# Performance work log

Measured on AMD Instinct MI355X. Metric: run time of the kernel, lower is better.

## Reference

```python
import jax, jax.numpy as jnp
import numpy as np

B, K, T = 64, 256, 64      # batch, num_tokens (feature dim of e / Dense units), word tokens
DF, N = 768, 1024          # image feature channels, spatial regions


def setup_inputs() -> dict:
    key = jax.random.key(0)
    k1, k2, k3 = jax.random.split(key, 3)
    e = jax.random.normal(k1, (B, K, T), dtype=jnp.float32)
    f = jax.random.normal(k2, (B, DF, N), dtype=jnp.float32)
    # Dense(units=K) kernel/bias (Glorot-ish scale)
    W = jax.random.normal(k3, (DF, K), dtype=jnp.float32) / np.sqrt(DF)
    b = jnp.zeros((K,), dtype=jnp.float32)
    gamma = jnp.float32(5.0)  # DAMSM smoothing factor gamma1
    return {"e": e, "f": f, "gamma": gamma, "W": W, "b": b}


def reference(e, f, gamma, W, b):
    # v = transpose(Dense(transpose(f))): project image features Df -> K. [B,K,N]
    v = jnp.einsum('bdn,dk->bkn', f, W) + b[None, :, None]
    # attention scores between word tokens and regions: [B,T,N]
    s = jnp.einsum('bkt,bkn->btn', e, v)
    # gamma-scaled softmax over regions (axis=2)
    alpha = jax.nn.softmax(gamma * s, axis=2)
    # region-context vectors per token: [B,K,T]
    c = jnp.einsum('bkn,btn->bkt', v, alpha)
    # per-token feature norms (reduce over feature axis 1): [B,T]
    lc = jnp.sqrt(jnp.sum(c * c, axis=1))
    le = jnp.sqrt(jnp.sum(e * e, axis=1))
    # token-token cosine similarity: contract feature axis, normalize by outer(lc, le)
    cos = jnp.einsum('bki,bkj->bij', c, e) / (lc[:, :, None] * le[:, None, :])
    return cos
```

## Files before the change

kernel.cpp:

```cpp
#include <hip/hip_runtime.h>

#define B_  64
#define K_  256
#define T_  64
#define DF_ 768
#define N_  1024

typedef __attribute__((ext_vector_type(8))) short bf16x8;
typedef __attribute__((ext_vector_type(4))) float f32x4;

__device__ __forceinline__ unsigned short bf_rne(float x) {
    unsigned u = __float_as_uint(x);
    unsigned r = u + 0x7fffu + ((u >> 16) & 1u);
    return (unsigned short)(r >> 16);
}

__global__ __launch_bounds__(256) void prep_we(const float* __restrict__ W,
                                               const float* __restrict__ e,
                                               unsigned short* __restrict__ W_hi,
                                               unsigned short* __restrict__ W_lo,
                                               unsigned short* __restrict__ WT_hi,
                                               unsigned short* __restrict__ eT_hi,
                                               unsigned short* __restrict__ eT_lo) {
    int blk = blockIdx.x;
    if (blk < DF_) {
        int d = blk, k = threadIdx.x;
        float w = W[d * K_ + k];
        unsigned u = __float_as_uint(w);
        unsigned short hs = (unsigned short)(u >> 16);
        float hi = __uint_as_float(u & 0xffff0000u);
        W_hi[d * K_ + k]   = hs;
        W_lo[d * K_ + k]   = bf_rne(w - hi);
        WT_hi[k * DF_ + d] = hs;
    } else {
        int q = blk - DF_;
        int b = q >> 2, kq = q & 3;
        int t = threadIdx.x & 63, ko = threadIdx.x >> 6;
        const float* eb = e + (size_t)b * K_ * T_;
        unsigned short* eh = eT_hi + (size_t)b * T_ * K_;
        unsigned short* el = eT_lo + (size_t)b * T_ * K_;
#pragma unroll
        for (int i = 0; i < 16; i++) {
            int k = kq * 64 + ko * 16 + i;
            float x = eb[k * T_ + t];
            unsigned u = __float_as_uint(x);
            unsigned short hs = (unsigned short)(u >> 16);
            float hi = __uint_as_float(u & 0xffff0000u);
            eh[t * K_ + k] = hs;
            el[t * K_ + k] = bf_rne(x - hi);
        }
    }
}

__global__ __launch_bounds__(256, 2) void gemm_g(const unsigned short* __restrict__ eT_hi,
                                                 const unsigned short* __restrict__ eT_lo,
                                                 const unsigned short* __restrict__ W_hi,
                                                 const unsigned short* __restrict__ W_lo,
                                                 unsigned short* __restrict__ gT_hi,
                                                 unsigned short* __restrict__ gT_lo) {
    __shared__ unsigned short LeH[64 * 40], LeL[64 * 40];
    __shared__ unsigned short LwH[64 * 40], LwL[64 * 40];
    const int dblk = blockIdx.x * 64;
    const int b = blockIdx.y;
    const int tid = threadIdx.x;
    const int lane = tid & 63, w = tid >> 6, q = lane >> 4, l16 = lane & 15;

    const unsigned short* eh = eT_hi + (size_t)b * T_ * K_;
    const unsigned short* el = eT_lo + (size_t)b * T_ * K_;

    f32x4 acc[4];
#pragma unroll
    for (int i = 0; i < 4; i++) acc[i] = (f32x4)(0.f);

    const int tr = tid >> 2, c8 = (tid & 3) * 8;
    for (int k0 = 0; k0 < K_; k0 += 32) {
        *(uint4*)&LeH[tr * 40 + c8] = *(const uint4*)&eh[tr * K_ + k0 + c8];
        *(uint4*)&LeL[tr * 40 + c8] = *(const uint4*)&el[tr * K_ + k0 + c8];
        *(uint4*)&LwH[tr * 40 + c8] = *(const uint4*)&W_hi[(size_t)(dblk + tr) * K_ + k0 + c8];
        *(uint4*)&LwL[tr * 40 + c8] = *(const uint4*)&W_lo[(size_t)(dblk + tr) * K_ + k0 + c8];
        __syncthreads();
        bf16x8 aH[4], aL[4], bH, bL;
#pragma unroll
        for (int mt = 0; mt < 4; mt++) {
            aH[mt] = *(const bf16x8*)&LeH[(mt * 16 + l16) * 40 + q * 8];
            aL[mt] = *(const bf16x8*)&LeL[(mt * 16 + l16) * 40 + q * 8];
        }
        int dl = w * 16 + l16;
        bH = *(const bf16x8*)&LwH[dl * 40 + q * 8];
        bL = *(const bf16x8*)&LwL[dl * 40 + q * 8];
#pragma unroll
        for (int mt = 0; mt < 4; mt++) {
            acc[mt] = __builtin_amdgcn_mfma_f32_16x16x32_bf16(aH[mt], bH, acc[mt], 0, 0, 0);
            acc[mt] = __builtin_amdgcn_mfma_f32_16x16x32_bf16(aH[mt], bL, acc[mt], 0, 0, 0);
            acc[mt] = __builtin_amdgcn_mfma_f32_16x16x32_bf16(aL[mt], bH, acc[mt], 0, 0, 0);
        }
        __syncthreads();
    }

    unsigned short* gh = gT_hi + (size_t)b * T_ * DF_;
    unsigned short* gl = gT_lo + (size_t)b * T_ * DF_;
#pragma unroll
    for (int mt = 0; mt < 4; mt++)
#pragma unroll
        for (int r = 0; r < 4; r++) {
            float x = acc[mt][r];
            int t = mt * 16 + q * 4 + r;
            int d = dblk + w * 16 + l16;
            unsigned u = __float_as_uint(x);
            unsigned short hs = (unsigned short)(u >> 16);
            float hi = __uint_as_float(u & 0xffff0000u);
            gh[t * DF_ + d] = hs;
            gl[t * DF_ + d] = bf_rne(x - hi);
        }
}

__global__ __launch_bounds__(256, 2) void gemm_s(const unsigned short* __restrict__ gT_hi,
                                                 const unsigned short* __restrict__ gT_lo,
                                                 const float* __restrict__ f,
                                                 float* __restrict__ s) {
    __shared__ unsigned short LgH[64 * 40], LgL[64 * 40];
    __shared__ unsigned LfH[128 * 20], LfL[128 * 20];

    const int flat = blockIdx.x;
    const int b    = (flat & 7) * 8 + ((flat >> 3) & 7);
    const int nblk = (flat >> 6) * 128;
    const int tid = threadIdx.x;
    const int lane = tid & 63, w = tid >> 6, q = lane >> 4, l16 = lane & 15;

    const unsigned short* gh = gT_hi + (size_t)b * T_ * DF_;
    const unsigned short* gl = gT_lo + (size_t)b * T_ * DF_;

    f32x4 acc[4][2];
#pragma unroll
    for (int i = 0; i < 4; i++)
#pragma unroll
        for (int j = 0; j < 2; j++) acc[i][j] = (f32x4)(0.f);

    const int dp  = tid >> 4;
    const int nb  = (tid & 15) * 8;
    const int rot = tid & 7;
    const int tr = tid >> 2, c8 = (tid & 3) * 8;

    for (int d0 = 0; d0 < DF_; d0 += 32) {
        *(uint4*)&LgH[tr * 40 + c8] = *(const uint4*)&gh[tr * DF_ + d0 + c8];
        *(uint4*)&LgL[tr * 40 + c8] = *(const uint4*)&gl[tr * DF_ + d0 + c8];
        {
            const float* fp = f + ((size_t)b * DF_ + d0 + dp * 2) * N_ + nblk + nb;
            float4 x0 = *(const float4*)&fp[0];
            float4 x1 = *(const float4*)&fp[4];
            float4 y0 = *(const float4*)&fp[N_ + 0];
            float4 y1 = *(const float4*)&fp[N_ + 4];
            const float xs[8] = {x0.x, x0.y, x0.z, x0.w, x1.x, x1.y, x1.z, x1.w};
            const float ys[8] = {y0.x, y0.y, y0.z, y0.w, y1.x, y1.y, y1.z, y1.w};
#pragma unroll
            for (int jj = 0; jj < 8; jj++) {
                int j = (jj + rot) & 7;
                unsigned bx = __float_as_uint(xs[j]);
                unsigned by = __float_as_uint(ys[j]);
                unsigned hp = (bx >> 16) | (by & 0xffff0000u);
                float lx = xs[j] - __uint_as_float(bx & 0xffff0000u);
                float ly = ys[j] - __uint_as_float(by & 0xffff0000u);
                unsigned lp = (__float_as_uint(lx) >> 16) | (__float_as_uint(ly) & 0xffff0000u);
                LfH[(nb + j) * 20 + dp] = hp;
                LfL[(nb + j) * 20 + dp] = lp;
            }
        }
        __syncthreads();
        bf16x8 aH[4], aL[4], bH[2], bL[2];
#pragma unroll
        for (int mt = 0; mt < 4; mt++) {
            aH[mt] = *(const bf16x8*)&LgH[(mt * 16 + l16) * 40 + q * 8];
            aL[mt] = *(const bf16x8*)&LgL[(mt * 16 + l16) * 40 + q * 8];
        }
#pragma unroll
        for (int nt = 0; nt < 2; nt++) {
            int nl = w * 32 + nt * 16 + l16;
            bH[nt] = *(const bf16x8*)&((const unsigned short*)LfH)[nl * 40 + q * 8];
            bL[nt] = *(const bf16x8*)&((const unsigned short*)LfL)[nl * 40 + q * 8];
        }
#pragma unroll
        for (int mt = 0; mt < 4; mt++)
#pragma unroll
            for (int nt = 0; nt < 2; nt++) {
                acc[mt][nt] = __builtin_amdgcn_mfma_f32_16x16x32_bf16(aH[mt], bH[nt], acc[mt][nt], 0, 0, 0);
                acc[mt][nt] = __builtin_amdgcn_mfma_f32_16x16x32_bf16(aH[mt], bL[nt], acc[mt][nt], 0, 0, 0);
                acc[mt][nt] = __builtin_amdgcn_mfma_f32_16x16x32_bf16(aL[mt], bH[nt], acc[mt][nt], 0, 0, 0);
            }
        __syncthreads();
    }

    float* sb = s + (size_t)b * T_ * N_;
#pragma unroll
    for (int mt = 0; mt < 4; mt++)
#pragma unroll
        for (int nt = 0; nt < 2; nt++)
#pragma unroll
            for (int r = 0; r < 4; r++) {
                int t = mt * 16 + q * 4 + r;
                int n = nblk + w * 32 + nt * 16 + l16;
                sb[(size_t)t * N_ + n] = acc[mt][nt][r];
            }
}

__global__ __launch_bounds__(256) void softmax_k(const float* __restrict__ s,
                                                 unsigned short* __restrict__ alpha,
                                                 const float* __restrict__ gptr) {
    const float g = gptr[0];
    const float* row = s + (size_t)blockIdx.x * N_;
    unsigned short* arow = alpha + (size_t)blockIdx.x * N_;
    const int t = threadIdx.x;

    float4 x = *(const float4*)(row + t * 4);
    x.x *= g; x.y *= g; x.z *= g; x.w *= g;

    float m = fmaxf(fmaxf(x.x, x.y), fmaxf(x.z, x.w));
#pragma unroll
    for (int off = 32; off > 0; off >>= 1) m = fmaxf(m, __shfl_xor(m, off, 64));
    __shared__ float sm[4], ss[4];
    int wave = t >> 6;
    if ((t & 63) == 0) sm[wave] = m;
    __syncthreads();
    m = fmaxf(fmaxf(sm[0], sm[1]), fmaxf(sm[2], sm[3]));

    float e0 = __expf(x.x - m), e1 = __expf(x.y - m);
    float e2 = __expf(x.z - m), e3 = __expf(x.w - m);
    float sum = e0 + e1 + e2 + e3;
#pragma unroll
    for (int off = 32; off > 0; off >>= 1) sum += __shfl_xor(sum, off, 64);
    if ((t & 63) == 0) ss[wave] = sum;
    __syncthreads();
    sum = ss[0] + ss[1] + ss[2] + ss[3];
    float inv = 1.f / sum;
    unsigned p0 = (unsigned)bf_rne(e0 * inv) | ((unsigned)bf_rne(e1 * inv) << 16);
    unsigned p1 = (unsigned)bf_rne(e2 * inv) | ((unsigned)bf_rne(e3 * inv) << 16);
    uint2 o; o.x = p0; o.y = p1;
    *(uint2*)&arow[t * 4] = o;
}

__global__ __launch_bounds__(256, 2) void gemm_h(const float* __restrict__ f,
                                                 const unsigned short* __restrict__ alpha,
                                                 unsigned short* __restrict__ hT) {
    __shared__ unsigned short Lf[64 * 72];
    __shared__ unsigned short La[64 * 72];
    const int dblk = blockIdx.x * 64;
    const int b = blockIdx.y;
    const int tid = threadIdx.x;
    const int lane = tid & 63, w = tid >> 6, q = lane >> 4, l16 = lane & 15;

    const float* fb = f + (size_t)b * DF_ * N_;
    const unsigned short* ab = alpha + (size_t)b * T_ * N_;

    f32x4 acc[4];
#pragma unroll
    for (int i = 0; i < 4; i++) acc[i] = (f32x4)(0.f);

    const int fr_ = tid >> 2, fc = tid & 3;
    for (int n0 = 0; n0 < N_; n0 += 64) {
        const float* frp = fb + (size_t)(dblk + fr_) * N_ + n0 + fc * 16;
#pragma unroll
        for (int i = 0; i < 4; i++) {
            float4 x = *(const float4*)&frp[i * 4];
            unsigned p0 = (unsigned)bf_rne(x.x) | ((unsigned)bf_rne(x.y) << 16);
            unsigned p1 = (unsigned)bf_rne(x.z) | ((unsigned)bf_rne(x.w) << 16);
            uint2 o; o.x = p0; o.y = p1;
            *(uint2*)&Lf[fr_ * 72 + fc * 16 + i * 4] = o;
        }
#pragma unroll
        for (int l = 0; l < 2; l++) {
            int idx = tid * 2 + l;
            int r = idx >> 3, c8 = (idx & 7) * 8;
            *(uint4*)&La[r * 72 + c8] = *(const uint4*)&ab[(size_t)r * N_ + n0 + c8];
        }
        __syncthreads();
        bf16x8 af[2], bb[4][2];
#pragma unroll
        for (int kk = 0; kk < 2; kk++)
            af[kk] = *(const bf16x8*)&Lf[(w * 16 + l16) * 72 + kk * 32 + q * 8];
#pragma unroll
        for (int nt = 0; nt < 4; nt++)
#pragma unroll
            for (int kk = 0; kk < 2; kk++)
                bb[nt][kk] = *(const bf16x8*)&La[(nt * 16 + l16) * 72 + kk * 32 + q * 8];
#pragma unroll
        for (int nt = 0; nt < 4; nt++)
#pragma unroll
            for (int kk = 0; kk < 2; kk++)
                acc[nt] = __builtin_amdgcn_mfma_f32_16x16x32_bf16(af[kk], bb[nt][kk], acc[nt], 0, 0, 0);
        __syncthreads();
    }

    unsigned short* hb = hT + (size_t)b * T_ * DF_;
#pragma unroll
    for (int nt = 0; nt < 4; nt++)
#pragma unroll
        for (int r = 0; r < 4; r++) {
            int d = dblk + w * 16 + q * 4 + r;
            int t = nt * 16 + l16;
            hb[(size_t)t * DF_ + d] = bf_rne(acc[nt][r]);
        }
}

__global__ __launch_bounds__(256, 2) void gemm_c(const unsigned short* __restrict__ WT_hi,
                                                 const unsigned short* __restrict__ hT,
                                                 const float* __restrict__ bias,
                                                 float* __restrict__ c) {
    __shared__ unsigned short LW[64 * 72];
    __shared__ unsigned short Lh[64 * 72];
    const int kblk = blockIdx.x * 64;
    const int b = blockIdx.y;
    const int tid = threadIdx.x;
    const int lane = tid & 63, w = tid >> 6, q = lane >> 4, l16 = lane & 15;

    const unsigned short* hb = hT + (size_t)b * T_ * DF_;

    f32x4 acc[4];
#pragma unroll
    for (int i = 0; i < 4; i++) acc[i] = (f32x4)(0.f);

    for (int d0 = 0; d0 < DF_; d0 += 64) {
#pragma unroll
        for (int l = 0; l < 2; l++) {
            int idx = tid * 2 + l;
            int r = idx >> 3, c8 = (idx & 7) * 8;
            *(uint4*)&LW[r * 72 + c8] = *(const uint4*)&WT_hi[(size_t)(kblk + r) * DF_ + d0 + c8];
            *(uint4*)&Lh[r * 72 + c8] = *(const uint4*)&hb[(size_t)r * DF_ + d0 + c8];
        }
        __syncthreads();
        bf16x8 aw[2], bh[4][2];
#pragma unroll
        for (int kk = 0; kk < 2; kk++)
            aw[kk] = *(const bf16x8*)&LW[(w * 16 + l16) * 72 + kk * 32 + q * 8];
#pragma unroll
        for (int nt = 0; nt < 4; nt++)
#pragma unroll
            for (int kk = 0; kk < 2; kk++)
                bh[nt][kk] = *(const bf16x8*)&Lh[(nt * 16 + l16) * 72 + kk * 32 + q * 8];
#pragma unroll
        for (int nt = 0; nt < 4; nt++)
#pragma unroll
            for (int kk = 0; kk < 2; kk++)
                acc[nt] = __builtin_amdgcn_mfma_f32_16x16x32_bf16(aw[kk], bh[nt][kk], acc[nt], 0, 0, 0);
        __syncthreads();
    }

    float* cb = c + (size_t)b * K_ * T_;
#pragma unroll
    for (int nt = 0; nt < 4; nt++)
#pragma unroll
        for (int r = 0; r < 4; r++) {
            int k = kblk + w * 16 + q * 4 + r;
            int t = nt * 16 + l16;
            cb[(size_t)k * T_ + t] = acc[nt][r] + bias[k];
        }
}

__global__ __launch_bounds__(256) void cos_k(const float* __restrict__ c,
                                             const float* __restrict__ e,
                                             float* __restrict__ out) {
    const int iq = threadIdx.x >> 6;
    const int i = blockIdx.x * 4 + iq;
    const int b = blockIdx.y;
    const int j = threadIdx.x & 63;
    const float* cb = c + (size_t)b * K_ * T_;
    const float* eb = e + (size_t)b * K_ * T_;

    float dot = 0.f, se = 0.f, sc = 0.f;
#pragma unroll 8
    for (int k = 0; k < K_; k++) {
        float cv = cb[(size_t)k * T_ + i];
        float ev = eb[(size_t)k * T_ + j];
        dot += cv * ev;
        se  += ev * ev;
        sc  += cv * cv;
    }
    out[((size_t)b * T_ + i) * T_ + j] = dot * rsqrtf(sc * se);
}

extern "C" void kernel_launch(void* const* d_in, const int* in_sizes, int n_in,
                              void* d_out, int out_size, void* d_ws, size_t ws_size,
                              hipStream_t stream) {
    const float* e     = (const float*)d_in[0];
    const float* f     = (const float*)d_in[1];
    const float* gamma = (const float*)d_in[2];
    const float* W     = (const float*)d_in[3];
    const float* bias  = (const float*)d_in[4];
    float* out = (float*)d_out;

    char* p = (char*)d_ws;
    unsigned short* W_hi  = (unsigned short*)p; p += (size_t)DF_ * K_ * 2;
    unsigned short* W_lo  = (unsigned short*)p; p += (size_t)DF_ * K_ * 2;
    unsigned short* WT_hi = (unsigned short*)p; p += (size_t)DF_ * K_ * 2;
    unsigned short* eT_hi = (unsigned short*)p; p += (size_t)B_ * T_ * K_ * 2;
    unsigned short* eT_lo = (unsigned short*)p; p += (size_t)B_ * T_ * K_ * 2;
    unsigned short* gT_hi = (unsigned short*)p; p += (size_t)B_ * T_ * DF_ * 2;
    unsigned short* gT_lo = (unsigned short*)p; p += (size_t)B_ * T_ * DF_ * 2;
    float*          s     = (float*)p;          p += (size_t)B_ * T_ * N_ * 4;
    unsigned short* alpha = (unsigned short*)p; p += (size_t)B_ * T_ * N_ * 2;
    unsigned short* hT    = (unsigned short*)p; p += (size_t)B_ * T_ * DF_ * 2;
    float*          c     = (float*)p;          p += (size_t)B_ * K_ * T_ * 4;

    prep_we <<<dim3(DF_ + 256),     256, 0, stream>>>(W, e, W_hi, W_lo, WT_hi, eT_hi, eT_lo);
    gemm_g  <<<dim3(DF_ / 64, B_),  256, 0, stream>>>(eT_hi, eT_lo, W_hi, W_lo, gT_hi, gT_lo);
    gemm_s  <<<dim3(512),           256, 0, stream>>>(gT_hi, gT_lo, f, s);
    softmax_k<<<dim3(B_ * T_),      256, 0, stream>>>(s, alpha, gamma);
    gemm_h  <<<dim3(DF_ / 64, B_),  256, 0, stream>>>(f, alpha, hT);
    gemm_c  <<<dim3(K_ / 64, B_),   256, 0, stream>>>(WT_hi, hT, bias, c);
    cos_k   <<<dim3(T_ / 4, B_),    256, 0, stream>>>(c, e, out);
}
```

Baseline: 383.5 us.

## Register-prefetch global loads in GEMM kernels and use one wave per softmax row

Adds register double-buffering to the gemm_g, gemm_s, gemm_h and gemm_c main loops. Each loop loads the next tile's global data into registers while the current tile is computed from LDS, so global memory latency is overlapped with MFMA work. The softmax kernel now assigns one wavefront per row, four rows per block, which removes the LDS cross-wave reductions and block barriers. Launch bounds for gemm_g and gemm_h are raised to 3 blocks per CU. The extra live prefetch registers may force spills or lower occupancy under that tighter register budget.

```diff
diff --git a/kernel.cpp b/kernel.cpp
--- a/kernel.cpp
+++ b/kernel.cpp
@@ -52,7 +52,7 @@
     }
 }
 
-__global__ __launch_bounds__(256, 2) void gemm_g(const unsigned short* __restrict__ eT_hi,
+__global__ __launch_bounds__(256, 3) void gemm_g(const unsigned short* __restrict__ eT_hi,
                                                  const unsigned short* __restrict__ eT_lo,
                                                  const unsigned short* __restrict__ W_hi,
                                                  const unsigned short* __restrict__ W_lo,
@@ -73,12 +73,27 @@
     for (int i = 0; i < 4; i++) acc[i] = (f32x4)(0.f);
 
     const int tr = tid >> 2, c8 = (tid & 3) * 8;
-    for (int k0 = 0; k0 < K_; k0 += 32) {
-        *(uint4*)&LeH[tr * 40 + c8] = *(const uint4*)&eh[tr * K_ + k0 + c8];
-        *(uint4*)&LeL[tr * 40 + c8] = *(const uint4*)&el[tr * K_ + k0 + c8];
-        *(uint4*)&LwH[tr * 40 + c8] = *(const uint4*)&W_hi[(size_t)(dblk + tr) * K_ + k0 + c8];
-        *(uint4*)&LwL[tr * 40 + c8] = *(const uint4*)&W_lo[(size_t)(dblk + tr) * K_ + k0 + c8];
-        __syncthreads();
+    const unsigned short* ehp = eh + (size_t)tr * K_ + c8;
+    const unsigned short* elp = el + (size_t)tr * K_ + c8;
+    const unsigned short* whp = W_hi + (size_t)(dblk + tr) * K_ + c8;
+    const unsigned short* wlp = W_lo + (size_t)(dblk + tr) * K_ + c8;
+
+    struct GSet { uint4 eH, eL, wH, wL; };
+    GSet A, Bv;
+
+    auto gload = [&](GSet& S, int k0) {
+        S.eH = *(const uint4*)&ehp[k0];
+        S.eL = *(const uint4*)&elp[k0];
+        S.wH = *(const uint4*)&whp[k0];
+        S.wL = *(const uint4*)&wlp[k0];
+    };
+    auto gstore = [&](const GSet& S) {
+        *(uint4*)&LeH[tr * 40 + c8] = S.eH;
+        *(uint4*)&LeL[tr * 40 + c8] = S.eL;
+        *(uint4*)&LwH[tr * 40 + c8] = S.wH;
+        *(uint4*)&LwL[tr * 40 + c8] = S.wL;
+    };
+    auto gcomp = [&]() {
         bf16x8 aH[4], aL[4], bH, bL;
 #pragma unroll
         for (int mt = 0; mt < 4; mt++) {
@@ -94,6 +109,19 @@
             acc[mt] = __builtin_amdgcn_mfma_f32_16x16x32_bf16(aH[mt], bL, acc[mt], 0, 0, 0);
             acc[mt] = __builtin_amdgcn_mfma_f32_16x16x32_bf16(aL[mt], bH, acc[mt], 0, 0, 0);
         }
+    };
+
+    gload(A, 0);
+    for (int k0 = 0; k0 < K_; k0 += 64) {
+        gload(Bv, k0 + 32);
+        gstore(A);
+        __syncthreads();
+        gcomp();
+        __syncthreads();
+        if (k0 + 64 < K_) gload(A, k0 + 64);
+        gstore(Bv);
+        __syncthreads();
+        gcomp();
         __syncthreads();
     }
 
@@ -141,31 +169,41 @@
     const int rot = tid & 7;
     const int tr = tid >> 2, c8 = (tid & 3) * 8;
 
-    for (int d0 = 0; d0 < DF_; d0 += 32) {
-        *(uint4*)&LgH[tr * 40 + c8] = *(const uint4*)&gh[tr * DF_ + d0 + c8];
-        *(uint4*)&LgL[tr * 40 + c8] = *(const uint4*)&gl[tr * DF_ + d0 + c8];
-        {
-            const float* fp = f + ((size_t)b * DF_ + d0 + dp * 2) * N_ + nblk + nb;
-            float4 x0 = *(const float4*)&fp[0];
-            float4 x1 = *(const float4*)&fp[4];
-            float4 y0 = *(const float4*)&fp[N_ + 0];
-            float4 y1 = *(const float4*)&fp[N_ + 4];
-            const float xs[8] = {x0.x, x0.y, x0.z, x0.w, x1.x, x1.y, x1.z, x1.w};
-            const float ys[8] = {y0.x, y0.y, y0.z, y0.w, y1.x, y1.y, y1.z, y1.w};
-#pragma unroll
-            for (int jj = 0; jj < 8; jj++) {
-                int j = (jj + rot) & 7;
-                unsigned bx = __float_as_uint(xs[j]);
-                unsigned by = __float_as_uint(ys[j]);
-                unsigned hp = (bx >> 16) | (by & 0xffff0000u);
-                float lx = xs[j] - __uint_as_float(bx & 0xffff0000u);
-                float ly = ys[j] - __uint_as_float(by & 0xffff0000u);
-                unsigned lp = (__float_as_uint(lx) >> 16) | (__float_as_uint(ly) & 0xffff0000u);
-                LfH[(nb + j) * 20 + dp] = hp;
-                LfL[(nb + j) * 20 + dp] = lp;
-            }
-        }
-        __syncthreads();
+    const float* fbase = f + ((size_t)b * DF_ + dp * 2) * N_ + nblk + nb;
+    const unsigned short* ghp = gh + (size_t)tr * DF_ + c8;
+    const unsigned short* glp = gl + (size_t)tr * DF_ + c8;
+
+    struct FSet { float4 x0, x1, y0, y1; uint4 gH, gL; };
+    FSet A, Bv;
+
+    auto sload = [&](FSet& S, int d0) {
+        const float* fp = fbase + (size_t)d0 * N_;
+        S.x0 = *(const float4*)&fp[0];
+        S.x1 = *(const float4*)&fp[4];
+        S.y0 = *(const float4*)&fp[N_ + 0];
+        S.y1 = *(const float4*)&fp[N_ + 4];
+        S.gH = *(const uint4*)&ghp[d0];
+        S.gL = *(const uint4*)&glp[d0];
+    };
+    auto sstore = [&](const FSet& S) {
+        *(uint4*)&LgH[tr * 40 + c8] = S.gH;
+        *(uint4*)&LgL[tr * 40 + c8] = S.gL;
+        const float xs[8] = {S.x0.x, S.x0.y, S.x0.z, S.x0.w, S.x1.x, S.x1.y, S.x1.z, S.x1.w};
+        const float ys[8] = {S.y0.x, S.y0.y, S.y0.z, S.y0.w, S.y1.x, S.y1.y, S.y1.z, S.y1.w};
+#pragma unroll
+        for (int jj = 0; jj < 8; jj++) {
+            int j = (jj + rot) & 7;
+            unsigned bx = __float_as_uint(xs[j]);
+            unsigned by = __float_as_uint(ys[j]);
+            unsigned hp = (bx >> 16) | (by & 0xffff0000u);
+            float lx = xs[j] - __uint_as_float(bx & 0xffff0000u);
+            float ly = ys[j] - __uint_as_float(by & 0xffff0000u);
+            unsigned lp = (__float_as_uint(lx) >> 16) | (__float_as_uint(ly) & 0xffff0000u);
+            LfH[(nb + j) * 20 + dp] = hp;
+            LfL[(nb + j) * 20 + dp] = lp;
+        }
+    };
+    auto scomp = [&]() {
         bf16x8 aH[4], aL[4], bH[2], bL[2];
 #pragma unroll
         for (int mt = 0; mt < 4; mt++) {
@@ -186,6 +224,19 @@
                 acc[mt][nt] = __builtin_amdgcn_mfma_f32_16x16x32_bf16(aH[mt], bL[nt], acc[mt][nt], 0, 0, 0);
                 acc[mt][nt] = __builtin_amdgcn_mfma_f32_16x16x32_bf16(aL[mt], bH[nt], acc[mt][nt], 0, 0, 0);
             }
+    };
+
+    sload(A, 0);
+    for (int d0 = 0; d0 < DF_; d0 += 64) {
+        sload(Bv, d0 + 32);
+        sstore(A);
+        __syncthreads();
+        scomp();
+        __syncthreads();
+        if (d0 + 64 < DF_) sload(A, d0 + 64);
+        sstore(Bv);
+        __syncthreads();
+        scomp();
         __syncthreads();
     }
 
@@ -206,38 +257,47 @@
                                                  unsigned short* __restrict__ alpha,
                                                  const float* __restrict__ gptr) {
     const float g = gptr[0];
-    const float* row = s + (size_t)blockIdx.x * N_;
-    unsigned short* arow = alpha + (size_t)blockIdx.x * N_;
-    const int t = threadIdx.x;
-
-    float4 x = *(const float4*)(row + t * 4);
-    x.x *= g; x.y *= g; x.z *= g; x.w *= g;
-
-    float m = fmaxf(fmaxf(x.x, x.y), fmaxf(x.z, x.w));
+    const int row_id = blockIdx.x * 4 + (threadIdx.x >> 6);
+    const int lane = threadIdx.x & 63;
+    const float* row = s + (size_t)row_id * N_;
+    unsigned short* arow = alpha + (size_t)row_id * N_;
+
+    float4 x[4];
+#pragma unroll
+    for (int i = 0; i < 4; i++) {
+        x[i] = *(const float4*)(row + i * 256 + lane * 4);
+        x[i].x *= g; x[i].y *= g; x[i].z *= g; x[i].w *= g;
+    }
+    float m = x[0].x;
+#pragma unroll
+    for (int i = 0; i < 4; i++)
+        m = fmaxf(m, fmaxf(fmaxf(x[i].x, x[i].y), fmaxf(x[i].z, x[i].w)));
 #pragma unroll
     for (int off = 32; off > 0; off >>= 1) m = fmaxf(m, __shfl_xor(m, off, 64));
-    __shared__ float sm[4], ss[4];
-    int wave = t >> 6;
-    if ((t & 63) == 0) sm[wave] = m;
-    __syncthreads();
-    m = fmaxf(fmaxf(sm[0], sm[1]), fmaxf(sm[2], sm[3]));
-
-    float e0 = __expf(x.x - m), e1 = __expf(x.y - m);
-    float e2 = __expf(x.z - m), e3 = __expf(x.w - m);
-    float sum = e0 + e1 + e2 + e3;
+
+    float ev[16];
+    float sum = 0.f;
+#pragma unroll
+    for (int i = 0; i < 4; i++) {
+        ev[i * 4 + 0] = __expf(x[i].x - m);
+        ev[i * 4 + 1] = __expf(x[i].y - m);
+        ev[i * 4 + 2] = __expf(x[i].z - m);
+        ev[i * 4 + 3] = __expf(x[i].w - m);
+        sum += ev[i * 4 + 0] + ev[i * 4 + 1] + ev[i * 4 + 2] + ev[i * 4 + 3];
+    }
 #pragma unroll
     for (int off = 32; off > 0; off >>= 1) sum += __shfl_xor(sum, off, 64);
-    if ((t & 63) == 0) ss[wave] = sum;
-    __syncthreads();
-    sum = ss[0] + ss[1] + ss[2] + ss[3];
     float inv = 1.f / sum;
-    unsigned p0 = (unsigned)bf_rne(e0 * inv) | ((unsigned)bf_rne(e1 * inv) << 16);
-    unsigned p1 = (unsigned)bf_rne(e2 * inv) | ((unsigned)bf_rne(e3 * inv) << 16);
-    uint2 o; o.x = p0; o.y = p1;
-    *(uint2*)&arow[t * 4] = o;
-}
-
-__global__ __launch_bounds__(256, 2) void gemm_h(const float* __restrict__ f,
+#pragma unroll
+    for (int i = 0; i < 4; i++) {
+        unsigned p0 = (unsigned)bf_rne(ev[i * 4 + 0] * inv) | ((unsigned)bf_rne(ev[i * 4 + 1] * inv) << 16);
+        unsigned p1 = (unsigned)bf_rne(ev[i * 4 + 2] * inv) | ((unsigned)bf_rne(ev[i * 4 + 3] * inv) << 16);
+        uint2 o; o.x = p0; o.y = p1;
+        *(uint2*)&arow[i * 256 + lane * 4] = o;
+    }
+}
+
+__global__ __launch_bounds__(256, 3) void gemm_h(const float* __restrict__ f,
                                                  const unsigned short* __restrict__ alpha,
                                                  unsigned short* __restrict__ hT) {
     __shared__ unsigned short Lf[64 * 72];
@@ -255,23 +315,36 @@
     for (int i = 0; i < 4; i++) acc[i] = (f32x4)(0.f);
 
     const int fr_ = tid >> 2, fc = tid & 3;
-    for (int n0 = 0; n0 < N_; n0 += 64) {
-        const float* frp = fb + (size_t)(dblk + fr_) * N_ + n0 + fc * 16;
+    const float* frbase = fb + (size_t)(dblk + fr_) * N_ + fc * 16;
+    const int ar = tid >> 2, ac = (tid & 3) * 16;
+    const unsigned short* abase = ab + (size_t)ar * N_ + ac;
+
+    struct HSet { float4 f0, f1, f2, f3; uint4 a0, a1; };
+    HSet A, Bv;
+
+    auto hload = [&](HSet& S, int n0) {
+        const float* fp = frbase + n0;
+        S.f0 = *(const float4*)&fp[0];
+        S.f1 = *(const float4*)&fp[4];
+        S.f2 = *(const float4*)&fp[8];
+        S.f3 = *(const float4*)&fp[12];
+        S.a0 = *(const uint4*)&abase[n0];
+        S.a1 = *(const uint4*)&abase[n0 + 8];
+    };
+    auto hstore = [&](const HSet& S) {
+        const float4 fx[4] = {S.f0, S.f1, S.f2, S.f3};
 #pragma unroll
         for (int i = 0; i < 4; i++) {
-            float4 x = *(const float4*)&frp[i * 4];
+            float4 x = fx[i];
             unsigned p0 = (unsigned)bf_rne(x.x) | ((unsigned)bf_rne(x.y) << 16);
             unsigned p1 = (unsigned)bf_rne(x.z) | ((unsigned)bf_rne(x.w) << 16);
             uint2 o; o.x = p0; o.y = p1;
             *(uint2*)&Lf[fr_ * 72 + fc * 16 + i * 4] = o;
         }
-#pragma unroll
-        for (int l = 0; l < 2; l++) {
-            int idx = tid * 2 + l;
-            int r = idx >> 3, c8 = (idx & 7) * 8;
-            *(uint4*)&La[r * 72 + c8] = *(const uint4*)&ab[(size_t)r * N_ + n0 + c8];
-        }
-        __syncthreads();
+        *(uint4*)&La[ar * 72 + ac] = S.a0;
+        *(uint4*)&La[ar * 72 + ac + 8] = S.a1;
+    };
+    auto hcomp = [&]() {
         bf16x8 af[2], bb[4][2];
 #pragma unroll
         for (int kk = 0; kk < 2; kk++)
@@ -286,6 +359,19 @@
 #pragma unroll
             for (int kk = 0; kk < 2; kk++)
                 acc[nt] = __builtin_amdgcn_mfma_f32_16x16x32_bf16(af[kk], bb[nt][kk], acc[nt], 0, 0, 0);
+    };
+
+    hload(A, 0);
+    for (int n0 = 0; n0 < N_; n0 += 128) {
+        hload(Bv, n0 + 64);
+        hstore(A);
+        __syncthreads();
+        hcomp();
+        __syncthreads();
+        if (n0 + 128 < N_) hload(A, n0 + 128);
+        hstore(Bv);
+        __syncthreads();
+        hcomp();
         __syncthreads();
     }
 
@@ -317,15 +403,26 @@
 #pragma unroll
     for (int i = 0; i < 4; i++) acc[i] = (f32x4)(0.f);
 
-    for (int d0 = 0; d0 < DF_; d0 += 64) {
-#pragma unroll
-        for (int l = 0; l < 2; l++) {
-            int idx = tid * 2 + l;
-            int r = idx >> 3, c8 = (idx & 7) * 8;
-            *(uint4*)&LW[r * 72 + c8] = *(const uint4*)&WT_hi[(size_t)(kblk + r) * DF_ + d0 + c8];
-            *(uint4*)&Lh[r * 72 + c8] = *(const uint4*)&hb[(size_t)r * DF_ + d0 + c8];
-        }
-        __syncthreads();
+    const int r_ = tid >> 2, cc = (tid & 3) * 16;
+    const unsigned short* wbase = WT_hi + (size_t)(kblk + r_) * DF_ + cc;
+    const unsigned short* hbase = hb + (size_t)r_ * DF_ + cc;
+
+    struct CSet { uint4 w0, w1, h0, h1; };
+    CSet A, Bv;
+
+    auto cload = [&](CSet& S, int d0) {
+        S.w0 = *(const uint4*)&wbase[d0];
+        S.w1 = *(const uint4*)&wbase[d0 + 8];
+        S.h0 = *(const uint4*)&hbase[d0];
+        S.h1 = *(const uint4*)&hbase[d0 + 8];
+    };
+    auto cstore = [&](const CSet& S) {
+        *(uint4*)&LW[r_ * 72 + cc]     = S.w0;
+        *(uint4*)&LW[r_ * 72 + cc + 8] = S.w1;
+        *(uint4*)&Lh[r_ * 72 + cc]     = S.h0;
+        *(uint4*)&Lh[r_ * 72 + cc + 8] = S.h1;
+    };
+    auto ccomp = [&]() {
         bf16x8 aw[2], bh[4][2];
 #pragma unroll
         for (int kk = 0; kk < 2; kk++)
@@ -340,6 +437,19 @@
 #pragma unroll
             for (int kk = 0; kk < 2; kk++)
                 acc[nt] = __builtin_amdgcn_mfma_f32_16x16x32_bf16(aw[kk], bh[nt][kk], acc[nt], 0, 0, 0);
+    };
+
+    cload(A, 0);
+    for (int d0 = 0; d0 < DF_; d0 += 128) {
+        cload(Bv, d0 + 64);
+        cstore(A);
+        __syncthreads();
+        ccomp();
+        __syncthreads();
+        if (d0 + 128 < DF_) cload(A, d0 + 128);
+        cstore(Bv);
+        __syncthreads();
+        ccomp();
         __syncthreads();
     }
 
@@ -399,11 +509,11 @@
     unsigned short* hT    = (unsigned short*)p; p += (size_t)B_ * T_ * DF_ * 2;
     float*          c     = (float*)p;          p += (size_t)B_ * K_ * T_ * 4;
 
-    prep_we <<<dim3(DF_ + 256),     256, 0, stream>>>(W, e, W_hi, W_lo, WT_hi, eT_hi, eT_lo);
-    gemm_g  <<<dim3(DF_ / 64, B_),  256, 0, stream>>>(eT_hi, eT_lo, W_hi, W_lo, gT_hi, gT_lo);
-    gemm_s  <<<dim3(512),           256, 0, stream>>>(gT_hi, gT_lo, f, s);
-    softmax_k<<<dim3(B_ * T_),      256, 0, stream>>>(s, alpha, gamma);
-    gemm_h  <<<dim3(DF_ / 64, B_),  256, 0, stream>>>(f, alpha, hT);
-    gemm_c  <<<dim3(K_ / 64, B_),   256, 0, stream>>>(WT_hi, hT, bias, c);
-    cos_k   <<<dim3(T_ / 4, B_),    256, 0, stream>>>(c, e, out);
-}
+    prep_we <<<dim3(DF_ + 256),      256, 0, stream>>>(W, e, W_hi, W_lo, WT_hi, eT_hi, eT_lo);
+    gemm_g  <<<dim3(DF_ / 64, B_),   256, 0, stream>>>(eT_hi, eT_lo, W_hi, W_lo, gT_hi, gT_lo);
+    gemm_s  <<<dim3(512),            256, 0, stream>>>(gT_hi, gT_lo, f, s);
+    softmax_k<<<dim3(B_ * T_ / 4),   256, 0, stream>>>(s, alpha, gamma);
+    gemm_h  <<<dim3(DF_ / 64, B_),   256, 0, stream>>>(f, alpha, hT);
+    gemm_c  <<<dim3(K_ / 64, B_),    256, 0, stream>>>(WT_hi, hT, bias, c);
+    cos_k   <<<dim3(T_ / 4, B_),     256, 0, stream>>>(c, e, out);
+}
```

Result: slower. 417.2 us (+8.8%).

## Double-buffer LDS in gemm_s and gemm_h; one wave per softmax row

Applied to the files above, without the earlier changes.

gemm_s and gemm_h now use double-buffered shared memory with register prefetch. The global loads for the next K-tile are issued before the MFMA work on the current tile, and each iteration needs one barrier instead of two. softmax_k now handles one row per wavefront, four rows per block, so reductions use only shuffles and no shared-memory barriers. The change doubles LDS use and raises register pressure, which could lower occupancy in the GEMMs.

```diff
diff --git a/kernel.cpp b/kernel.cpp
--- a/kernel.cpp
+++ b/kernel.cpp
@@ -118,8 +118,8 @@
                                                  const unsigned short* __restrict__ gT_lo,
                                                  const float* __restrict__ f,
                                                  float* __restrict__ s) {
-    __shared__ unsigned short LgH[64 * 40], LgL[64 * 40];
-    __shared__ unsigned LfH[128 * 20], LfL[128 * 20];
+    __shared__ unsigned short LgH[2][64 * 40], LgL[2][64 * 40];
+    __shared__ unsigned LfH[2][128 * 20], LfL[2][128 * 20];
 
     const int flat = blockIdx.x;
     const int b    = (flat & 7) * 8 + ((flat >> 3) & 7);
@@ -141,42 +141,52 @@
     const int rot = tid & 7;
     const int tr = tid >> 2, c8 = (tid & 3) * 8;
 
-    for (int d0 = 0; d0 < DF_; d0 += 32) {
-        *(uint4*)&LgH[tr * 40 + c8] = *(const uint4*)&gh[tr * DF_ + d0 + c8];
-        *(uint4*)&LgL[tr * 40 + c8] = *(const uint4*)&gl[tr * DF_ + d0 + c8];
-        {
-            const float* fp = f + ((size_t)b * DF_ + d0 + dp * 2) * N_ + nblk + nb;
-            float4 x0 = *(const float4*)&fp[0];
-            float4 x1 = *(const float4*)&fp[4];
-            float4 y0 = *(const float4*)&fp[N_ + 0];
-            float4 y1 = *(const float4*)&fp[N_ + 4];
-            const float xs[8] = {x0.x, x0.y, x0.z, x0.w, x1.x, x1.y, x1.z, x1.w};
-            const float ys[8] = {y0.x, y0.y, y0.z, y0.w, y1.x, y1.y, y1.z, y1.w};
-#pragma unroll
-            for (int jj = 0; jj < 8; jj++) {
-                int j = (jj + rot) & 7;
-                unsigned bx = __float_as_uint(xs[j]);
-                unsigned by = __float_as_uint(ys[j]);
-                unsigned hp = (bx >> 16) | (by & 0xffff0000u);
-                float lx = xs[j] - __uint_as_float(bx & 0xffff0000u);
-                float ly = ys[j] - __uint_as_float(by & 0xffff0000u);
-                unsigned lp = (__float_as_uint(lx) >> 16) | (__float_as_uint(ly) & 0xffff0000u);
-                LfH[(nb + j) * 20 + dp] = hp;
-                LfL[(nb + j) * 20 + dp] = lp;
-            }
-        }
-        __syncthreads();
+    const float* fbase = f + ((size_t)b * DF_ + dp * 2) * N_ + nblk + nb;
+    const unsigned short* ghp = gh + (size_t)tr * DF_ + c8;
+    const unsigned short* glp = gl + (size_t)tr * DF_ + c8;
+
+    float4 px0, px1, py0, py1;
+    uint4 pgH, pgL;
+
+    auto sload = [&](int d0) {
+        const float* fp = fbase + (size_t)d0 * N_;
+        px0 = *(const float4*)&fp[0];
+        px1 = *(const float4*)&fp[4];
+        py0 = *(const float4*)&fp[N_ + 0];
+        py1 = *(const float4*)&fp[N_ + 4];
+        pgH = *(const uint4*)&ghp[d0];
+        pgL = *(const uint4*)&glp[d0];
+    };
+    auto sstore = [&](int buf) {
+        *(uint4*)&LgH[buf][tr * 40 + c8] = pgH;
+        *(uint4*)&LgL[buf][tr * 40 + c8] = pgL;
+        const float xs[8] = {px0.x, px0.y, px0.z, px0.w, px1.x, px1.y, px1.z, px1.w};
+        const float ys[8] = {py0.x, py0.y, py0.z, py0.w, py1.x, py1.y, py1.z, py1.w};
+#pragma unroll
+        for (int jj = 0; jj < 8; jj++) {
+            int j = (jj + rot) & 7;
+            unsigned bx = __float_as_uint(xs[j]);
+            unsigned by = __float_as_uint(ys[j]);
+            unsigned hp = (bx >> 16) | (by & 0xffff0000u);
+            float lx = xs[j] - __uint_as_float(bx & 0xffff0000u);
+            float ly = ys[j] - __uint_as_float(by & 0xffff0000u);
+            unsigned lp = (__float_as_uint(lx) >> 16) | (__float_as_uint(ly) & 0xffff0000u);
+            LfH[buf][(nb + j) * 20 + dp] = hp;
+            LfL[buf][(nb + j) * 20 + dp] = lp;
+        }
+    };
+    auto scomp = [&](int buf) {
         bf16x8 aH[4], aL[4], bH[2], bL[2];
 #pragma unroll
         for (int mt = 0; mt < 4; mt++) {
-            aH[mt] = *(const bf16x8*)&LgH[(mt * 16 + l16) * 40 + q * 8];
-            aL[mt] = *(const bf16x8*)&LgL[(mt * 16 + l16) * 40 + q * 8];
+            aH[mt] = *(const bf16x8*)&LgH[buf][(mt * 16 + l16) * 40 + q * 8];
+            aL[mt] = *(const bf16x8*)&LgL[buf][(mt * 16 + l16) * 40 + q * 8];
         }
 #pragma unroll
         for (int nt = 0; nt < 2; nt++) {
             int nl = w * 32 + nt * 16 + l16;
-            bH[nt] = *(const bf16x8*)&((const unsigned short*)LfH)[nl * 40 + q * 8];
-            bL[nt] = *(const bf16x8*)&((const unsigned short*)LfL)[nl * 40 + q * 8];
+            bH[nt] = *(const bf16x8*)&((const unsigned short*)LfH[buf])[nl * 40 + q * 8];
+            bL[nt] = *(const bf16x8*)&((const unsigned short*)LfL[buf])[nl * 40 + q * 8];
         }
 #pragma unroll
         for (int mt = 0; mt < 4; mt++)
@@ -186,8 +196,20 @@
                 acc[mt][nt] = __builtin_amdgcn_mfma_f32_16x16x32_bf16(aH[mt], bL[nt], acc[mt][nt], 0, 0, 0);
                 acc[mt][nt] = __builtin_amdgcn_mfma_f32_16x16x32_bf16(aL[mt], bH[nt], acc[mt][nt], 0, 0, 0);
             }
-        __syncthreads();
-    }
+    };
+
+    sload(0);
+    sstore(0);
+    __syncthreads();
+    int cur = 0;
+    for (int d0 = 0; d0 < DF_ - 32; d0 += 32) {
+        sload(d0 + 32);
+        scomp(cur);
+        sstore(cur ^ 1);
+        __syncthreads();
+        cur ^= 1;
+    }
+    scomp(cur);
 
     float* sb = s + (size_t)b * T_ * N_;
 #pragma unroll
@@ -206,42 +228,51 @@
                                                  unsigned short* __restrict__ alpha,
                                                  const float* __restrict__ gptr) {
     const float g = gptr[0];
-    const float* row = s + (size_t)blockIdx.x * N_;
-    unsigned short* arow = alpha + (size_t)blockIdx.x * N_;
-    const int t = threadIdx.x;
-
-    float4 x = *(const float4*)(row + t * 4);
-    x.x *= g; x.y *= g; x.z *= g; x.w *= g;
-
-    float m = fmaxf(fmaxf(x.x, x.y), fmaxf(x.z, x.w));
+    const int row_id = blockIdx.x * 4 + (threadIdx.x >> 6);
+    const int lane = threadIdx.x & 63;
+    const float* row = s + (size_t)row_id * N_;
+    unsigned short* arow = alpha + (size_t)row_id * N_;
+
+    float4 x[4];
+#pragma unroll
+    for (int i = 0; i < 4; i++) {
+        x[i] = *(const float4*)(row + i * 256 + lane * 4);
+        x[i].x *= g; x[i].y *= g; x[i].z *= g; x[i].w *= g;
+    }
+    float m = x[0].x;
+#pragma unroll
+    for (int i = 0; i < 4; i++)
+        m = fmaxf(m, fmaxf(fmaxf(x[i].x, x[i].y), fmaxf(x[i].z, x[i].w)));
 #pragma unroll
     for (int off = 32; off > 0; off >>= 1) m = fmaxf(m, __shfl_xor(m, off, 64));
-    __shared__ float sm[4], ss[4];
-    int wave = t >> 6;
-    if ((t & 63) == 0) sm[wave] = m;
-    __syncthreads();
-    m = fmaxf(fmaxf(sm[0], sm[1]), fmaxf(sm[2], sm[3]));
-
-    float e0 = __expf(x.x - m), e1 = __expf(x.y - m);
-    float e2 = __expf(x.z - m), e3 = __expf(x.w - m);
-    float sum = e0 + e1 + e2 + e3;
+
+    float ev[16];
+    float sum = 0.f;
+#pragma unroll
+    for (int i = 0; i < 4; i++) {
+        ev[i * 4 + 0] = __expf(x[i].x - m);
+        ev[i * 4 + 1] = __expf(x[i].y - m);
+        ev[i * 4 + 2] = __expf(x[i].z - m);
+        ev[i * 4 + 3] = __expf(x[i].w - m);
+        sum += ev[i * 4 + 0] + ev[i * 4 + 1] + ev[i * 4 + 2] + ev[i * 4 + 3];
+    }
 #pragma unroll
     for (int off = 32; off > 0; off >>= 1) sum += __shfl_xor(sum, off, 64);
-    if ((t & 63) == 0) ss[wave] = sum;
-    __syncthreads();
-    sum = ss[0] + ss[1] + ss[2] + ss[3];
     float inv = 1.f / sum;
-    unsigned p0 = (unsigned)bf_rne(e0 * inv) | ((unsigned)bf_rne(e1 * inv) << 16);
-    unsigned p1 = (unsigned)bf_rne(e2 * inv) | ((unsigned)bf_rne(e3 * inv) << 16);
-    uint2 o; o.x = p0; o.y = p1;
-    *(uint2*)&arow[t * 4] = o;
+#pragma unroll
+    for (int i = 0; i < 4; i++) {
+        unsigned p0 = (unsigned)bf_rne(ev[i * 4 + 0] * inv) | ((unsigned)bf_rne(ev[i * 4 + 1] * inv) << 16);
+        unsigned p1 = (unsigned)bf_rne(ev[i * 4 + 2] * inv) | ((unsigned)bf_rne(ev[i * 4 + 3] * inv) << 16);
+        uint2 o; o.x = p0; o.y = p1;
+        *(uint2*)&arow[i * 256 + lane * 4] = o;
+    }
 }
 
 __global__ __launch_bounds__(256, 2) void gemm_h(const float* __restrict__ f,
                                                  const unsigned short* __restrict__ alpha,
                                                  unsigned short* __restrict__ hT) {
-    __shared__ unsigned short Lf[64 * 72];
-    __shared__ unsigned short La[64 * 72];
+    __shared__ unsigned short Lf[2][64 * 72];
+    __shared__ unsigned short La[2][64 * 72];
     const int dblk = blockIdx.x * 64;
     const int b = blockIdx.y;
     const int tid = threadIdx.x;
@@ -255,39 +286,63 @@
     for (int i = 0; i < 4; i++) acc[i] = (f32x4)(0.f);
 
     const int fr_ = tid >> 2, fc = tid & 3;
-    for (int n0 = 0; n0 < N_; n0 += 64) {
-        const float* frp = fb + (size_t)(dblk + fr_) * N_ + n0 + fc * 16;
+    const float* frbase = fb + (size_t)(dblk + fr_) * N_ + fc * 16;
+    const unsigned short* abase = ab + (size_t)fr_ * N_ + fc * 16;
+
+    float4 pf0, pf1, pf2, pf3;
+    uint4 pa0, pa1;
+
+    auto hload = [&](int n0) {
+        const float* fp = frbase + n0;
+        pf0 = *(const float4*)&fp[0];
+        pf1 = *(const float4*)&fp[4];
+        pf2 = *(const float4*)&fp[8];
+        pf3 = *(const float4*)&fp[12];
+        pa0 = *(const uint4*)&abase[n0];
+        pa1 = *(const uint4*)&abase[n0 + 8];
+    };
+    auto hstore = [&](int buf) {
+        const float4 fx[4] = {pf0, pf1, pf2, pf3};
 #pragma unroll
         for (int i = 0; i < 4; i++) {
-            float4 x = *(const float4*)&frp[i * 4];
+            float4 x = fx[i];
             unsigned p0 = (unsigned)bf_rne(x.x) | ((unsigned)bf_rne(x.y) << 16);
             unsigned p1 = (unsigned)bf_rne(x.z) | ((unsigned)bf_rne(x.w) << 16);
             uint2 o; o.x = p0; o.y = p1;
-            *(uint2*)&Lf[fr_ * 72 + fc * 16 + i * 4] = o;
-        }
-#pragma unroll
-        for (int l = 0; l < 2; l++) {
-            int idx = tid * 2 + l;
-            int r = idx >> 3, c8 = (idx & 7) * 8;
-            *(uint4*)&La[r * 72 + c8] = *(const uint4*)&ab[(size_t)r * N_ + n0 + c8];
-        }
-        __syncthreads();
+            *(uint2*)&Lf[buf][fr_ * 72 + fc * 16 + i * 4] = o;
+        }
+        *(uint4*)&La[buf][fr_ * 72 + fc * 16]     = pa0;
+        *(uint4*)&La[buf][fr_ * 72 + fc * 16 + 8] = pa1;
+    };
+    auto hcomp = [&](int buf) {
         bf16x8 af[2], bb[4][2];
 #pragma unroll
         for (int kk = 0; kk < 2; kk++)
-            af[kk] = *(const bf16x8*)&Lf[(w * 16 + l16) * 72 + kk * 32 + q * 8];
+            af[kk] = *(const bf16x8*)&Lf[buf][(w * 16 + l16) * 72 + kk * 32 + q * 8];
 #pragma unroll
         for (int nt = 0; nt < 4; nt++)
 #pragma unroll
             for (int kk = 0; kk < 2; kk++)
-                bb[nt][kk] = *(const bf16x8*)&La[(nt * 16 + l16) * 72 + kk * 32 + q * 8];
+                bb[nt][kk] = *(const bf16x8*)&La[buf][(nt * 16 + l16) * 72 + kk * 32 + q * 8];
 #pragma unroll
         for (int nt = 0; nt < 4; nt++)
 #pragma unroll
             for (int kk = 0; kk < 2; kk++)
                 acc[nt] = __builtin_amdgcn_mfma_f32_16x16x32_bf16(af[kk], bb[nt][kk], acc[nt], 0, 0, 0);
-        __syncthreads();
-    }
+    };
+
+    hload(0);
+    hstore(0);
+    __syncthreads();
+    int cur = 0;
+    for (int n0 = 0; n0 < N_ - 64; n0 += 64) {
+        hload(n0 + 64);
+        hcomp(cur);
+        hstore(cur ^ 1);
+        __syncthreads();
+        cur ^= 1;
+    }
+    hcomp(cur);
 
     unsigned short* hb = hT + (size_t)b * T_ * DF_;
 #pragma unroll
@@ -399,11 +454,11 @@
     unsigned short* hT    = (unsigned short*)p; p += (size_t)B_ * T_ * DF_ * 2;
     float*          c     = (float*)p;          p += (size_t)B_ * K_ * T_ * 4;
 
-    prep_we <<<dim3(DF_ + 256),     256, 0, stream>>>(W, e, W_hi, W_lo, WT_hi, eT_hi, eT_lo);
-    gemm_g  <<<dim3(DF_ / 64, B_),  256, 0, stream>>>(eT_hi, eT_lo, W_hi, W_lo, gT_hi, gT_lo);
-    gemm_s  <<<dim3(512),           256, 0, stream>>>(gT_hi, gT_lo, f, s);
-    softmax_k<<<dim3(B_ * T_),      256, 0, stream>>>(s, alpha, gamma);
-    gemm_h  <<<dim3(DF_ / 64, B_),  256, 0, stream>>>(f, alpha, hT);
-    gemm_c  <<<dim3(K_ / 64, B_),   256, 0, stream>>>(WT_hi, hT, bias, c);
-    cos_k   <<<dim3(T_ / 4, B_),    256, 0, stream>>>(c, e, out);
-}
+    prep_we <<<dim3(DF_ + 256),      256, 0, stream>>>(W, e, W_hi, W_lo, WT_hi, eT_hi, eT_lo);
+    gemm_g  <<<dim3(DF_ / 64, B_),   256, 0, stream>>>(eT_hi, eT_lo, W_hi, W_lo, gT_hi, gT_lo);
+    gemm_s  <<<dim3(512),            256, 0, stream>>>(gT_hi, gT_lo, f, s);
+    softmax_k<<<dim3(B_ * T_ / 4),   256, 0, stream>>>(s, alpha, gamma);
+    gemm_h  <<<dim3(DF_ / 64, B_),   256, 0, stream>>>(f, alpha, hT);
+    gemm_c  <<<dim3(K_ / 64, B_),    256, 0, stream>>>(WT_hi, hT, bias, c);
+    cos_k   <<<dim3(T_ / 4, B_),     256, 0, stream>>>(c, e, out);
+}
```

Result: faster. 374.9 us (-2.2%).
